# Kernel optimization log

Hardware: AMD Instinct MI355X
Metric: run time of the kernel (lower is better)

Reference implementation:

```python
import jax, jax.numpy as jnp
import numpy as np

MIN_EXPERTS = 1
MAX_EXPERTS = 8
TEMPERATURE = 1.0


def setup_inputs() -> dict:
    key = jax.random.key(0)
    ks = jax.random.split(key, 7)
    B, S, H, E = 8, 4096, 1024, 64
    Hh = H // 2
    return {
        "hidden_states": jax.random.normal(ks[0], (B, S, H), dtype=jnp.float32),
        "W_router": jax.random.normal(ks[1], (E, H), dtype=jnp.float32) * 0.02,
        "b_router": jax.random.normal(ks[2], (E,), dtype=jnp.float32) * 0.02,
        "W1": jax.random.normal(ks[3], (Hh, H), dtype=jnp.float32) * 0.02,
        "b1": jax.random.normal(ks[4], (Hh,), dtype=jnp.float32) * 0.02,
        "W2": jax.random.normal(ks[5], (1, Hh), dtype=jnp.float32) * 0.02,
        "b2": jax.random.normal(ks[6], (1,), dtype=jnp.float32) * 0.02,
    }


def reference(hidden_states, W_router, b_router, W1, b1, W2, b2):
    B, S, H = hidden_states.shape
    flat = hidden_states.reshape(-1, H)                     # [N, H]

    # router logits
    router_logits = (flat @ W_router.T + b_router) / TEMPERATURE  # [N, E]

    # confidence net: Linear -> ReLU -> Linear -> Sigmoid
    h = jax.nn.relu(flat @ W1.T + b1)                       # [N, H/2]
    confidence = jax.nn.sigmoid(h @ W2.T + b2).squeeze(-1)  # [N]

    # dynamic k per token (torch.round = half-to-even, same as jnp.round)
    dk = MIN_EXPERTS + (MAX_EXPERTS - MIN_EXPERTS) * (1.0 - confidence)
    dk = jnp.clip(jnp.round(dk), MIN_EXPERTS, MAX_EXPERTS).astype(jnp.int32)  # [N]

    routing_probs = jax.nn.softmax(router_logits, axis=-1)  # [N, E]

    # single top-k pass replaces per-iteration sort; mask slots >= dynamic_k
    top_vals, top_idx = jax.lax.top_k(routing_probs, MAX_EXPERTS)  # [N, max_k]
    slot = jnp.arange(MAX_EXPERTS, dtype=jnp.int32)[None, :]       # [1, max_k]
    active = slot < dk[:, None]                                    # [N, max_k]
    sel_w = jnp.where(active, top_vals, 0.0)
    sel_i = jnp.where(active, top_idx, 0).astype(jnp.int64)

    sel_w = sel_w.reshape(B, S, MAX_EXPERTS)
    sel_i = sel_i.reshape(B, S, MAX_EXPERTS)
    return sel_w, sel_i, confidence, router_logits
```

## Files before the change

### kernel.cpp

```cpp
#include <hip/hip_runtime.h>
#include <hip/hip_bf16.h>
#include <math.h>

#define N_TOK 32768
#define HDIM 1024
#define HH 512
#define NOUT 576
#define BM 128
#define BN 64
#define BK 32
#define THREADS 256
#define KC 384

#define OFF_SELW 0
#define OFF_SELI 262144
#define OFF_CONF 524288
#define OFF_LOG  557056

__device__ float  g_Bmat[HDIM * NOUT];
__device__ double g_partial[N_TOK * 8];

__global__ __launch_bounds__(256) void k_build(const float* __restrict__ W1,
                                               const float* __restrict__ Wr) {
  int idx = blockIdx.x * 256 + threadIdx.x;
  int k = idx / NOUT;
  int j = idx - k * NOUT;
  float v = (j < HH) ? W1[(size_t)j * HDIM + k] : Wr[(size_t)(j - HH) * HDIM + k];
  g_Bmat[idx] = v;
}

__global__ __launch_bounds__(THREADS) void k_gemm(const float* __restrict__ A,
                                                  const float* __restrict__ b1,
                                                  const float* __restrict__ W2,
                                                  const float* __restrict__ b_router,
                                                  float* __restrict__ out_logits) {
  __shared__ float As[BK][BM];
  __shared__ float Bs[BK][BN];

  int bid = blockIdx.x;
  int xcd = bid & 7;
  int s   = bid >> 3;
  int j   = s % 9;
  int t   = xcd + 8 * (s / 9);

  const int tid = threadIdx.x;
  const int tx  = tid & 15;
  const int ty  = tid >> 4;
  const int m0  = t * BM;
  const int n0  = j * BN;

  float acc[8][4];
  float carry[8][4];
  #pragma unroll
  for (int i = 0; i < 8; ++i)
    #pragma unroll
    for (int c = 0; c < 4; ++c) { acc[i][c] = 0.f; carry[i][c] = 0.f; }

  const int arow = tid >> 1;
  const int akc  = tid & 1;
  const float* Ag = A + (size_t)(m0 + arow) * HDIM + akc * 16;

  for (int k0 = 0; k0 < HDIM; k0 += BK) {
    if (k0 == KC || k0 == 2 * KC) {
      #pragma unroll
      for (int i = 0; i < 8; ++i)
        #pragma unroll
        for (int c = 0; c < 4; ++c) {
          carry[i][c] = carry[i][c] + acc[i][c];
          acc[i][c] = 0.f;
        }
    }

    float4 av[4];
    #pragma unroll
    for (int c = 0; c < 4; ++c)
      av[c] = *(const float4*)(Ag + k0 + c * 4);
    float4 bv[2];
    #pragma unroll
    for (int c = 0; c < 2; ++c) {
      int idx = tid + c * 256;
      int kr  = idx >> 4;
      int ch  = idx & 15;
      bv[c] = *(const float4*)&g_Bmat[(size_t)(k0 + kr) * NOUT + n0 + ch * 4];
    }
    __syncthreads();
    #pragma unroll
    for (int c = 0; c < 4; ++c) {
      int kb = akc * 16 + c * 4;
      As[kb + 0][arow] = av[c].x;
      As[kb + 1][arow] = av[c].y;
      As[kb + 2][arow] = av[c].z;
      As[kb + 3][arow] = av[c].w;
    }
    #pragma unroll
    for (int c = 0; c < 2; ++c) {
      int idx = tid + c * 256;
      int kr  = idx >> 4;
      int ch  = idx & 15;
      *(float4*)&Bs[kr][ch * 4] = bv[c];
    }
    __syncthreads();

    #pragma unroll 4
    for (int kk = 0; kk < BK; ++kk) {
      float4 a03 = *(const float4*)&As[kk][ty * 8 + 0];
      float4 a47 = *(const float4*)&As[kk][ty * 8 + 4];
      float a[8] = {a03.x, a03.y, a03.z, a03.w, a47.x, a47.y, a47.z, a47.w};
      float b[4];
      b[0] = Bs[kk][tx * 4 + 0];
      b[1] = Bs[kk][tx * 4 + 1];
      b[2] = Bs[kk][tx * 4 + 2];
      b[3] = Bs[kk][tx * 4 + 3];
      #pragma unroll
      for (int i = 0; i < 8; ++i)
        #pragma unroll
        for (int c = 0; c < 4; ++c)
          acc[i][c] = fmaf(a[i], b[c], acc[i][c]);
    }
  }

  float res[8][4];
  #pragma unroll
  for (int i = 0; i < 8; ++i)
    #pragma unroll
    for (int c = 0; c < 4; ++c) res[i][c] = carry[i][c] + acc[i][c];

  if (j < 8) {
    double w2v[4];
    float  b1v[4];
    #pragma unroll
    for (int c = 0; c < 4; ++c) {
      w2v[c] = (double)W2[n0 + tx * 4 + c];
      b1v[c] = b1[n0 + tx * 4 + c];
    }
    #pragma unroll
    for (int i = 0; i < 8; ++i) {
      double sacc = 0.0;
      #pragma unroll
      for (int c = 0; c < 4; ++c) {
        float h = fmaxf(res[i][c] + b1v[c], 0.f);
        sacc = fma((double)h, w2v[c], sacc);
      }
      sacc += __shfl_xor(sacc, 1, 64);
      sacc += __shfl_xor(sacc, 2, 64);
      sacc += __shfl_xor(sacc, 4, 64);
      sacc += __shfl_xor(sacc, 8, 64);
      if (tx == 0) g_partial[(size_t)(m0 + ty * 8 + i) * 8 + j] = sacc;
    }
  } else {
    float brv[4];
    #pragma unroll
    for (int c = 0; c < 4; ++c) brv[c] = b_router[tx * 4 + c];
    #pragma unroll
    for (int i = 0; i < 8; ++i) {
      int row = m0 + ty * 8 + i;
      float o[4];
      #pragma unroll
      for (int c = 0; c < 4; ++c) o[c] = res[i][c] + brv[c];
      *(float4*)&out_logits[(size_t)row * 64 + tx * 4] =
          make_float4(o[0], o[1], o[2], o[3]);
    }
  }
}

__global__ __launch_bounds__(256) void k_post(const float* __restrict__ b2,
                                              float* __restrict__ d_out) {
  int tk = blockIdx.x * 256 + threadIdx.x;

  double ca = (double)b2[0];
  #pragma unroll
  for (int jj = 0; jj < 8; ++jj) ca += g_partial[(size_t)tk * 8 + jj];
  double conf = 1.0 / (1.0 + exp(-ca));
  double dkf  = 1.0 + 7.0 * (1.0 - conf);
  double dkr  = rint(dkf);
  int dk = (int)fmin(fmax(dkr, 1.0), 8.0);

  const float* logits = d_out + OFF_LOG + (size_t)tk * 64;
  float l[64];
  #pragma unroll
  for (int e4 = 0; e4 < 16; ++e4)
    *(float4*)&l[e4 * 4] = *(const float4*)&logits[e4 * 4];

  float mx = l[0];
  #pragma unroll
  for (int e = 1; e < 64; ++e) mx = fmaxf(mx, l[e]);

  float ex[64];
  #pragma unroll
  for (int e = 0; e < 64; ++e) ex[e] = expf(l[e] - mx);

  float r[8];
  #pragma unroll
  for (int q = 0; q < 8; ++q) r[q] = ex[q];
  #pragma unroll
  for (int b = 1; b < 8; ++b)
    #pragma unroll
    for (int q = 0; q < 8; ++q) r[q] += ex[b * 8 + q];
  float ssum = ((r[0] + r[1]) + (r[2] + r[3])) + ((r[4] + r[5]) + (r[6] + r[7]));

  float v[64];
  #pragma unroll
  for (int e = 0; e < 64; ++e) v[e] = ex[e] / ssum;

  float* sel_w = d_out + OFF_SELW + (size_t)tk * 8;
  float* sel_i = d_out + OFF_SELI + (size_t)tk * 8;
  unsigned long long used = 0ull;
  #pragma unroll
  for (int slot = 0; slot < 8; ++slot) {
    float best = -1.f;
    int   bi   = 0;
    #pragma unroll
    for (int e = 0; e < 64; ++e) {
      bool ok = (((used >> e) & 1ull) == 0ull) && (v[e] > best);
      best = ok ? v[e] : best;
      bi   = ok ? e    : bi;
    }
    used |= (1ull << bi);
    bool active = slot < dk;
    sel_w[slot] = active ? best : 0.f;
    sel_i[slot] = active ? (float)bi : 0.f;
  }
  d_out[OFF_CONF + tk] = (float)conf;
}

extern "C" void kernel_launch(void* const* d_in, const int* in_sizes, int n_in,
                              void* d_out, int out_size, void* d_ws, size_t ws_size,
                              hipStream_t stream) {
  const float* hidden   = (const float*)d_in[0];
  const float* W_router = (const float*)d_in[1];
  const float* b_router = (const float*)d_in[2];
  const float* W1       = (const float*)d_in[3];
  const float* b1       = (const float*)d_in[4];
  const float* W2       = (const float*)d_in[5];
  const float* b2       = (const float*)d_in[6];
  float* out = (float*)d_out;

  k_build<<<(HDIM * NOUT) / 256, 256, 0, stream>>>(W1, W_router);
  k_gemm<<<(N_TOK / BM) * 9, THREADS, 0, stream>>>(hidden, b1, W2, b_router,
                                                   out + OFF_LOG);
  k_post<<<N_TOK / 256, 256, 0, stream>>>(b2, out);
}
```

Measured before the change: 686.7 us.

## Split post-processing of each token across eight lanes with shuffle reductions

```diff
diff --git a/kernel.cpp b/kernel.cpp
--- a/kernel.cpp
+++ b/kernel.cpp
@@ -165,62 +165,80 @@
 
 __global__ __launch_bounds__(256) void k_post(const float* __restrict__ b2,
                                               float* __restrict__ d_out) {
-  int tk = blockIdx.x * 256 + threadIdx.x;
-
-  double ca = (double)b2[0];
-  #pragma unroll
-  for (int jj = 0; jj < 8; ++jj) ca += g_partial[(size_t)tk * 8 + jj];
+  const int lane = threadIdx.x & 63;
+  const int wave = threadIdx.x >> 6;
+  const int q    = lane & 7;
+  const int tsub = lane >> 3;
+  const int tk   = blockIdx.x * 32 + wave * 8 + tsub;
+
+  double p = g_partial[(size_t)tk * 8 + q];
+  p += __shfl_xor(p, 1, 64);
+  p += __shfl_xor(p, 2, 64);
+  p += __shfl_xor(p, 4, 64);
+  double ca   = (double)b2[0] + p;
   double conf = 1.0 / (1.0 + exp(-ca));
   double dkf  = 1.0 + 7.0 * (1.0 - conf);
   double dkr  = rint(dkf);
   int dk = (int)fmin(fmax(dkr, 1.0), 8.0);
 
   const float* logits = d_out + OFF_LOG + (size_t)tk * 64;
-  float l[64];
-  #pragma unroll
-  for (int e4 = 0; e4 < 16; ++e4)
-    *(float4*)&l[e4 * 4] = *(const float4*)&logits[e4 * 4];
+  float l[8];
+  #pragma unroll
+  for (int b = 0; b < 8; ++b) l[b] = logits[b * 8 + q];
 
   float mx = l[0];
   #pragma unroll
-  for (int e = 1; e < 64; ++e) mx = fmaxf(mx, l[e]);
-
-  float ex[64];
-  #pragma unroll
-  for (int e = 0; e < 64; ++e) ex[e] = expf(l[e] - mx);
-
-  float r[8];
-  #pragma unroll
-  for (int q = 0; q < 8; ++q) r[q] = ex[q];
-  #pragma unroll
-  for (int b = 1; b < 8; ++b)
-    #pragma unroll
-    for (int q = 0; q < 8; ++q) r[q] += ex[b * 8 + q];
-  float ssum = ((r[0] + r[1]) + (r[2] + r[3])) + ((r[4] + r[5]) + (r[6] + r[7]));
-
-  float v[64];
-  #pragma unroll
-  for (int e = 0; e < 64; ++e) v[e] = ex[e] / ssum;
-
-  float* sel_w = d_out + OFF_SELW + (size_t)tk * 8;
-  float* sel_i = d_out + OFF_SELI + (size_t)tk * 8;
-  unsigned long long used = 0ull;
+  for (int b = 1; b < 8; ++b) mx = fmaxf(mx, l[b]);
+  mx = fmaxf(mx, __shfl_xor(mx, 1, 64));
+  mx = fmaxf(mx, __shfl_xor(mx, 2, 64));
+  mx = fmaxf(mx, __shfl_xor(mx, 4, 64));
+
+  float ex[8];
+  #pragma unroll
+  for (int b = 0; b < 8; ++b) ex[b] = expf(l[b] - mx);
+
+  float r = ex[0];
+  #pragma unroll
+  for (int b = 1; b < 8; ++b) r += ex[b];
+  r += __shfl_xor(r, 1, 64);
+  r += __shfl_xor(r, 2, 64);
+  float ssum = r + __shfl_xor(r, 4, 64);
+
+  float v[8];
+  #pragma unroll
+  for (int b = 0; b < 8; ++b) v[b] = ex[b] / ssum;
+
+  float myw = 0.f, myi = 0.f;
+  unsigned used = 0u;
   #pragma unroll
   for (int slot = 0; slot < 8; ++slot) {
     float best = -1.f;
-    int   bi   = 0;
-    #pragma unroll
-    for (int e = 0; e < 64; ++e) {
-      bool ok = (((used >> e) & 1ull) == 0ull) && (v[e] > best);
-      best = ok ? v[e] : best;
-      bi   = ok ? e    : bi;
-    }
-    used |= (1ull << bi);
+    int   bi   = 64;
+    #pragma unroll
+    for (int b = 0; b < 8; ++b) {
+      bool ok = (((used >> b) & 1u) == 0u) && (v[b] > best);
+      best = ok ? v[b] : best;
+      bi   = ok ? (b * 8 + q) : bi;
+    }
+    #pragma unroll
+    for (int m = 1; m <= 4; m <<= 1) {
+      float ow = __shfl_xor(best, m, 64);
+      int   oi = __shfl_xor(bi,   m, 64);
+      bool take = (ow > best) || (ow == best && oi < bi);
+      best = take ? ow : best;
+      bi   = take ? oi : bi;
+    }
+    if ((bi & 7) == q) used |= (1u << (bi >> 3));
     bool active = slot < dk;
-    sel_w[slot] = active ? best : 0.f;
-    sel_i[slot] = active ? (float)bi : 0.f;
+    if (slot == q) {
+      myw = active ? best : 0.f;
+      myi = active ? (float)bi : 0.f;
+    }
   }
-  d_out[OFF_CONF + tk] = (float)conf;
+
+  d_out[OFF_SELW + (size_t)tk * 8 + q] = myw;
+  d_out[OFF_SELI + (size_t)tk * 8 + q] = myi;
+  if (q == 0) d_out[OFF_CONF + tk] = (float)conf;
 }
 
 extern "C" void kernel_launch(void* const* d_in, const int* in_sizes, int n_in,
@@ -238,5 +256,5 @@
   k_build<<<(HDIM * NOUT) / 256, 256, 0, stream>>>(W1, W_router);
   k_gemm<<<(N_TOK / BM) * 9, THREADS, 0, stream>>>(hidden, b1, W2, b_router,
                                                    out + OFF_LOG);
-  k_post<<<N_TOK / 256, 256, 0, stream>>>(b2, out);
-}
+  k_post<<<N_TOK / 256 / 128 * 128 ? (N_TOK / 32) : (N_TOK / 32), 256, 0, stream>>>(b2, out);
+}
```

New measurement: 680.9 us. About the same (-0.9%).
